# Kernel tuning notes

Hardware: AMD Instinct MI355X
Metric: run time of the kernel (lower is better)

## Reference

```python
import jax, jax.numpy as jnp
import numpy as np

C = 32
SHIFTS = (1, 2, 4)
KSIZE = 4  # trans_layer: kernel KSIZE+1, stride KSIZE, pad KSIZE//2
EPS_NORM = 1e-12
EPS_BN = 1e-5


def _make_diff_kernels(c):
    # 8 fixed 3x3 difference kernels, tiled per channel for depthwise conv.
    d1 = np.array([[[-1, 0, 0], [0, 1, 0], [0, 0, 0]],
                   [[0, -1, 0], [0, 1, 0], [0, 0, 0]],
                   [[0, 0, -1], [0, 1, 0], [0, 0, 0]],
                   [[0, 0, 0], [0, 1, -1], [0, 0, 0]]], dtype=np.float32)
    d1 = d1.reshape(4, 1, 3, 3)
    d2 = d1[:, :, ::-1, ::-1].copy()
    delta = np.concatenate([d1, d2], axis=0)          # [8,1,3,3]
    return jnp.asarray(np.tile(delta, (c, 1, 1, 1)))  # [8C,1,3,3]


DIFF_KERNELS = _make_diff_kernels(C)


def conv2d(x, w, stride=1, pad=0, dilation=1, groups=1):
    return jax.lax.conv_general_dilated(
        x, w, (stride, stride), [(pad, pad), (pad, pad)],
        rhs_dilation=(dilation, dilation),
        dimension_numbers=('NCHW', 'OIHW', 'NCHW'),
        feature_group_count=groups)


def l2norm(x, axis=-1):
    n = jnp.sqrt(jnp.sum(x * x, axis=axis, keepdims=True))
    return x / jnp.maximum(n, EPS_NORM)


def setup_inputs() -> dict:
    key = jax.random.key(0)
    ks = jax.random.split(key, 8)
    S = len(SHIFTS)
    return {
        'cen': jax.random.normal(ks[0], (2, C, 256, 256), jnp.float32),
        'trans_W': jax.random.normal(ks[1], (C, C, 5, 5), jnp.float32) * 0.05,
        'trans_b': jax.random.normal(ks[2], (C,), jnp.float32) * 0.05,
        'query_W': jax.random.normal(ks[3], (C, C, 1, 1), jnp.float32) * 0.05,
        'value_W': jax.random.normal(ks[4], (S, C, C, 1, 1), jnp.float32) * 0.05,
        'key_W': jax.random.normal(ks[5], (S, C, C, 1, 1), jnp.float32) * 0.05,
        'out_W': jax.random.normal(ks[6], (C, C, 1, 1), jnp.float32) * 0.05,
        'bn_gamma': jnp.ones((C,), jnp.float32),
        'bn_beta': jnp.zeros((C,), jnp.float32),
        'bn_mean': jnp.zeros((C,), jnp.float32),
        'bn_var': jnp.ones((C,), jnp.float32),
    }


def reference(cen, trans_W, trans_b, query_W, value_W, key_W, out_W,
              bn_gamma, bn_beta, bn_mean, bn_var):
    b, _, w, h = cen.shape
    S = len(SHIFTS)
    size = (w * h) // (KSIZE * KSIZE)

    # trans_layer: kernel KSIZE+1, stride KSIZE, pad KSIZE//2
    kv_cen = conv2d(cen, trans_W, stride=KSIZE, pad=KSIZE // 2) \
        + trans_b[None, :, None, None]

    keys, values = [], []
    for i, d in enumerate(SHIFTS):
        v = conv2d(cen, value_W[i])          # [b,C,w,h]
        k = conv2d(kv_cen, key_W[i])         # [b,C,w',h']
        # depthwise dilated difference conv -> 8 outputs per channel
        v = conv2d(v, DIFF_KERNELS, pad=d, dilation=d, groups=C)  # [b,8C,w,h]
        k = conv2d(k, DIFF_KERNELS, pad=d, dilation=d, groups=C)  # [b,8C,w',h']
        keys.append(k)
        values.append(v)

    querys = conv2d(kv_cen, query_W)  # [b,C,w',h']

    keys = jnp.stack(keys, axis=2).reshape(b, C, 8 * S, size)       # [b,C,8S,size]
    values = jnp.stack(values, axis=2).reshape(b, C, 8 * S, w * h)  # [b,C,8S,wh]

    keys = jnp.swapaxes(l2norm(keys, -1), -2, -1)        # [b,C,size,8S]
    querys = l2norm(querys.reshape(b, C, 1, size), -1)   # [b,C,1,size]

    score = jnp.matmul(querys, keys)   # [b,C,1,8S]  cosine sims
    score = l2norm(score, -1)
    out = jnp.matmul(score, values).reshape(b, C, w, h)

    # out_conv: 1x1 conv -> BN (eval mode, running stats) -> ReLU
    out = conv2d(out, out_W)
    inv = jax.lax.rsqrt(bn_var + EPS_BN)
    out = (out - bn_mean[None, :, None, None]) * (bn_gamma * inv)[None, :, None, None] \
        + bn_beta[None, :, None, None]
    return jax.nn.relu(out)
```

## Files before the change

### kernel.cpp

```cpp
#include <hip/hip_runtime.h>
#include <hip/hip_bf16.h>


#define CC 32
#define HW 256
#define KVW 64

__global__ __launch_bounds__(256, 2) void k1_trans(const float* __restrict__ cen,
                                                   const float* __restrict__ tW,
                                                   const float* __restrict__ tB,
                                                   float* __restrict__ kv) {
  int bid = blockIdx.x;
  int b = bid >> 8, cog = (bid >> 6) & 3, y = bid & 63;
  int tid = threadIdx.x;
  int x = tid & 63;
  int w = __builtin_amdgcn_readfirstlane(tid >> 6);
  int co0 = cog * 8 + w * 2;

  float acc0 = 0.f, acc1 = 0.f;
  const float4 z4 = {0.f, 0.f, 0.f, 0.f};

  int roff[5];
  bool rok[5];
#pragma unroll
  for (int r = 0; r < 5; r++) {
    int row = 4 * y - 2 + r;
    rok[r] = (row >= 0);
    roff[r] = (row < 0 ? 0 : row) * HW;
  }

  for (int ci = 0; ci < CC; ci += 4) {
    const float* pc[4];
#pragma unroll
    for (int c = 0; c < 4; c++) pc[c] = cen + (size_t)(b * CC + ci + c) * 65536 + 4 * x;
    float4 A[4][5], B[4][5];
#pragma unroll
    for (int c = 0; c < 4; c++) {
#pragma unroll
      for (int r = 0; r < 5; r++) {
        A[c][r] = (x > 0) ? *(const float4*)(pc[c] + roff[r] - 4) : z4;
        B[c][r] = *(const float4*)(pc[c] + roff[r]);
      }
    }
#pragma unroll
    for (int r = 0; r < 5; r++) {
      if (!rok[r]) continue;
#pragma unroll
      for (int c = 0; c < 4; c++) {
        const float* wa = tW + (co0 * CC + ci + c) * 25 + r * 5;
        const float* wb = wa + CC * 25;
        acc0 += wa[0] * A[c][r].z + wa[1] * A[c][r].w + wa[2] * B[c][r].x +
                wa[3] * B[c][r].y + wa[4] * B[c][r].z;
        acc1 += wb[0] * A[c][r].z + wb[1] * A[c][r].w + wb[2] * B[c][r].x +
                wb[3] * B[c][r].y + wb[4] * B[c][r].z;
      }
    }
  }
  kv[((b * CC + co0) * KVW + y) * KVW + x] = acc0 + tB[co0];
  kv[((b * CC + co0 + 1) * KVW + y) * KVW + x] = acc1 + tB[co0 + 1];
}

__device__ inline float wred64(float v) {
#pragma unroll
  for (int off = 1; off < 64; off <<= 1) v += __shfl_xor(v, off);
  return v;
}

__global__ __launch_bounds__(1024) void k2_scores(const float* __restrict__ kv,
                                                  const float* __restrict__ qW,
                                                  const float* __restrict__ kW,
                                                  float* __restrict__ scores) {
  __shared__ alignas(16) float kl[3][4096];
  __shared__ float wred[16][52];
  __shared__ float srl[24];
  int bc = blockIdx.x;
  int b = bc >> 5, c = bc & 31;
  int tid = threadIdx.x;
  int lane = tid & 63, w = tid >> 6;
  int xx = tid & 63;
  int ybase = tid >> 6;

  float qreg[4];
#pragma unroll
  for (int r = 0; r < 4; r++) {
    int px = r * 1024 + tid;
    float q = 0.f, k0 = 0.f, k1 = 0.f, k2 = 0.f;
    for (int ci = 0; ci < CC; ci++) {
      float val = kv[(b * CC + ci) * 4096 + px];
      q += qW[c * CC + ci] * val;
      k0 += kW[(0 * CC + c) * CC + ci] * val;
      k1 += kW[(1 * CC + c) * CC + ci] * val;
      k2 += kW[(2 * CC + c) * CC + ci] * val;
    }
    qreg[r] = q;
    kl[0][px] = k0;
    kl[1][px] = k1;
    kl[2][px] = k2;
  }
  __syncthreads();

  float q2 = 0.f;
#pragma unroll
  for (int r = 0; r < 4; r++) q2 += qreg[r] * qreg[r];
  q2 = wred64(q2);
  if (lane == 0) wred[w][48] = q2;

  constexpr int DYt[8] = {-1, -1, -1, 0, 1, 1, 1, 0};
  constexpr int DXt[8] = {-1, 0, 1, 1, 1, 0, -1, -1};
#pragma unroll
  for (int j = 0; j < 24; j++) {
    const int i = j >> 3, n = j & 7, d = 1 << i;
    const int dy = DYt[n], dx = DXt[n];
    int xn = xx + dx * d;
    bool xok = (xn >= 0 && xn < KVW);
    float dacc = 0.f, macc = 0.f;
#pragma unroll
    for (int r = 0; r < 4; r++) {
      int yy = r * 16 + ybase;
      int px = yy * KVW + xx;
      float kc = kl[i][px];
      int yn = yy + dy * d;
      float kn = (xok && yn >= 0 && yn < KVW) ? kl[i][yn * KVW + xn] : 0.f;
      float df = kc - kn;
      dacc += qreg[r] * df;
      macc += df * df;
    }
    dacc = wred64(dacc);
    macc = wred64(macc);
    if (lane == 0) {
      wred[w][j] = dacc;
      wred[w][24 + j] = macc;
    }
  }
  __syncthreads();
  if (tid < 24) {
    float D = 0.f, M = 0.f, Q2 = 0.f;
    for (int w2 = 0; w2 < 16; w2++) {
      D += wred[w2][tid];
      M += wred[w2][24 + tid];
      Q2 += wred[w2][48];
    }
    float sr = D / (fmaxf(sqrtf(M), 1e-12f) * fmaxf(sqrtf(Q2), 1e-12f));
    srl[tid] = sr;
  }
  __syncthreads();
  if (tid < 24) {
    float r2 = 0.f;
    for (int j = 0; j < 24; j++) r2 += srl[j] * srl[j];
    float s = srl[tid] / fmaxf(sqrtf(r2), 1e-12f);
    scores[(b * CC + c) * 24 + tid] = s;
  }
}

__global__ __launch_bounds__(256) void k3a_values(const float* __restrict__ cen,
                                                  const float* __restrict__ vW,
                                                  __hip_bfloat16* __restrict__ v) {
  int bid = blockIdx.x;
  int b = bid >> 9, blk = bid & 511;
  int tid = threadIdx.x;
  int lane = tid & 63;
  int cg = __builtin_amdgcn_readfirstlane(tid >> 6);
  int px = blk * 128 + lane * 2;

  float2 cr[CC];
#pragma unroll
  for (int ci = 0; ci < CC; ci++)
    cr[ci] = *(const float2*)(cen + (size_t)(b * CC + ci) * 65536 + px);

#pragma unroll
  for (int i = 0; i < 3; i++) {
#pragma unroll
    for (int cc = 0; cc < 8; cc++) {
      int c = cg * 8 + cc;
      const float* wp = vW + (i * CC + c) * CC;
      float a0 = 0.f, a1 = 0.f;
#pragma unroll
      for (int ci = 0; ci < CC; ci++) {
        a0 += wp[ci] * cr[ci].x;
        a1 += wp[ci] * cr[ci].y;
      }
      __hip_bfloat16 h0 = __float2bfloat16(a0);
      __hip_bfloat16 h1 = __float2bfloat16(a1);
      unsigned int pk = (unsigned int)(*(unsigned short*)&h0) |
                        ((unsigned int)(*(unsigned short*)&h1) << 16);
      *(unsigned int*)((unsigned short*)v + (((size_t)((i * 2 + b) * CC + c)) << 16) +
                       px) = pk;
    }
  }
}

__global__ __launch_bounds__(256) void k3b_combine(const __hip_bfloat16* __restrict__ v,
                                                   const float* __restrict__ scores,
                                                   const float* __restrict__ oW,
                                                   const float* __restrict__ gamma,
                                                   const float* __restrict__ beta,
                                                   const float* __restrict__ mean,
                                                   const float* __restrict__ var,
                                                   float* __restrict__ out) {
  __shared__ alignas(16) float vt[3 * 24 * 24 * 4];
  __shared__ alignas(16) float sl[27][32];
  __shared__ alignas(16) float owl[32][32];
  __shared__ float bns[32], bnb[32];

  int bid = blockIdx.x;
  int b = bid >> 8, tile = bid & 255;
  int ty = tile >> 4, tx = tile & 15;
  int tid = threadIdx.x;
  int ly = tid >> 4, lx = tid & 15;

  for (int f = tid; f < 24 * 32; f += 256) {
    int j = f >> 5, c = f & 31;
    sl[j][c] = scores[(b * CC + c) * 24 + j];
  }
  for (int f = tid; f < 1024; f += 256) owl[f >> 5][f & 31] = oW[f];
  if (tid < 32) {
    float inv = rsqrtf(var[tid] + 1e-5f);
    float sc = gamma[tid] * inv;
    bns[tid] = sc;
    bnb[tid] = beta[tid] - mean[tid] * sc;
  }
  __syncthreads();
  if (tid < 32) {
#pragma unroll
    for (int i = 0; i < 3; i++) {
      float s = 0.f;
      for (int n = 0; n < 8; n++) s += sl[i * 8 + n][tid];
      sl[24 + i][tid] = s;
    }
  }

  int ldsoff[4], pxoff[4], ibase[4];
  bool okp[4];
#pragma unroll
  for (int it = 0; it < 4; it++) {
    int p = tid + it * 256;
    bool act = (p < 864);
    int pp = act ? p : 0;
    int i = pp / 288;
    int rem = pp - i * 288;
    int r = rem / 12;
    int col = (rem - r * 12) * 2;
    int gy = ty * 16 + r - 4, gx = tx * 16 + col - 4;
    okp[it] = act && gy >= 0 && gy < HW && gx >= 0 && gx < HW;
    pxoff[it] = gy * HW + gx;
    ibase[it] = (i * 2 + b) * CC;
    ldsoff[it] = ((i * 24 + r) * 24 + col) * 4;
  }

  constexpr int DYt[8] = {-1, -1, -1, 0, 1, 1, 1, 0};
  constexpr int DXt[8] = {-1, 0, 1, 1, 1, 0, -1, -1};

  float acc[32];
#pragma unroll
  for (int co = 0; co < 32; co++) acc[co] = 0.f;

  unsigned int pf[4][4];
  const unsigned short* vs = (const unsigned short*)v;

#pragma unroll
  for (int it = 0; it < 4; it++)
#pragma unroll
    for (int cp = 0; cp < 4; cp++)
      pf[it][cp] = okp[it]
                       ? *(const unsigned int*)(vs + (((size_t)(ibase[it] + cp)) << 16) +
                                                pxoff[it])
                       : 0u;

  for (int cg = 0; cg < 8; cg++) {
    __syncthreads();
#pragma unroll
    for (int it = 0; it < 4; it++) {
      if (it == 3 && tid >= 96) continue;
      float4 lo, hi;
      lo.x = __uint_as_float(pf[it][0] << 16);
      lo.y = __uint_as_float(pf[it][1] << 16);
      lo.z = __uint_as_float(pf[it][2] << 16);
      lo.w = __uint_as_float(pf[it][3] << 16);
      hi.x = __uint_as_float(pf[it][0] & 0xffff0000u);
      hi.y = __uint_as_float(pf[it][1] & 0xffff0000u);
      hi.z = __uint_as_float(pf[it][2] & 0xffff0000u);
      hi.w = __uint_as_float(pf[it][3] & 0xffff0000u);
      *(float4*)&vt[ldsoff[it]] = lo;
      *(float4*)&vt[ldsoff[it] + 4] = hi;
    }
    if (cg < 7) {
      int cb = (cg + 1) * 4;
#pragma unroll
      for (int it = 0; it < 4; it++)
#pragma unroll
        for (int cp = 0; cp < 4; cp++)
          pf[it][cp] = okp[it] ? *(const unsigned int*)(vs +
                                                        (((size_t)(ibase[it] + cb + cp))
                                                         << 16) +
                                                        pxoff[it])
                               : 0u;
    }
    __syncthreads();

    float4 pre = {0.f, 0.f, 0.f, 0.f};
#pragma unroll
    for (int i = 0; i < 3; i++) {
      const int d = 1 << i;
      float4 S4 = *(const float4*)&sl[24 + i][cg * 4];
      float4 ctr = *(const float4*)&vt[((i * 24 + (ly + 4)) * 24 + (lx + 4)) * 4];
      pre.x += S4.x * ctr.x;
      pre.y += S4.y * ctr.y;
      pre.z += S4.z * ctr.z;
      pre.w += S4.w * ctr.w;
#pragma unroll
      for (int n = 0; n < 8; n++) {
        float4 sj = *(const float4*)&sl[i * 8 + n][cg * 4];
        float4 nb = *(const float4*)&vt[((i * 24 + (ly + 4 + DYt[n] * d)) * 24 +
                                         (lx + 4 + DXt[n] * d)) * 4];
        pre.x -= sj.x * nb.x;
        pre.y -= sj.y * nb.y;
        pre.z -= sj.z * nb.z;
        pre.w -= sj.w * nb.w;
      }
    }
#pragma unroll
    for (int co = 0; co < 32; co++) {
      float4 ow = *(const float4*)&owl[co][cg * 4];
      acc[co] += ow.x * pre.x + ow.y * pre.y + ow.z * pre.z + ow.w * pre.w;
    }
  }

  int gy = ty * 16 + ly, gx = tx * 16 + lx;
#pragma unroll
  for (int co = 0; co < 32; co++) {
    float val = acc[co] * bns[co] + bnb[co];
    out[((size_t)(b * CC + co) << 16) + gy * HW + gx] = fmaxf(val, 0.f);
  }
}

extern "C" void kernel_launch(void* const* d_in, const int* in_sizes, int n_in,
                              void* d_out, int out_size, void* d_ws, size_t ws_size,
                              hipStream_t stream) {
  const float* cen = (const float*)d_in[0];
  const float* trans_W = (const float*)d_in[1];
  const float* trans_b = (const float*)d_in[2];
  const float* query_W = (const float*)d_in[3];
  const float* value_W = (const float*)d_in[4];
  const float* key_W = (const float*)d_in[5];
  const float* out_W = (const float*)d_in[6];
  const float* bn_gamma = (const float*)d_in[7];
  const float* bn_beta = (const float*)d_in[8];
  const float* bn_mean = (const float*)d_in[9];
  const float* bn_var = (const float*)d_in[10];
  float* out = (float*)d_out;

  float* kv = (float*)d_ws;
  float* scores = (float*)((char*)d_ws + 524288);
  __hip_bfloat16* v = (__hip_bfloat16*)((char*)d_ws + 524288 + 8192);

  k1_trans<<<512, 256, 0, stream>>>(cen, trans_W, trans_b, kv);
  k2_scores<<<64, 1024, 0, stream>>>(kv, query_W, key_W, scores);
  k3a_values<<<1024, 256, 0, stream>>>(cen, value_W, v);
  k3b_combine<<<512, 256, 0, stream>>>(v, scores, out_W, bn_gamma, bn_beta, bn_mean,
                                       bn_var, out);
}
```

Baseline: 186.8 us.

## Split score kernel across shift index to raise block parallelism

The score computation is split into a partial kernel launched with one block per (batch, channel, shift), 192 blocks instead of 64, plus a small finalize kernel that combines the partial dot products and norms into normalized scores. This is meant to fill more compute units on the GPU, since 64 blocks of 1024 threads underuse the device. In exchange the query projection is recomputed three times, and an extra kernel launch and a workspace round trip are added.

After: 177.1 us. 1.05x faster.

```diff
diff --git a/kernel.cpp b/kernel.cpp
--- a/kernel.cpp
+++ b/kernel.cpp
@@ -66,14 +66,14 @@
   return v;
 }
 
-__global__ __launch_bounds__(1024) void k2_scores(const float* __restrict__ kv,
-                                                  const float* __restrict__ qW,
-                                                  const float* __restrict__ kW,
-                                                  float* __restrict__ scores) {
-  __shared__ alignas(16) float kl[3][4096];
-  __shared__ float wred[16][52];
-  __shared__ float srl[24];
-  int bc = blockIdx.x;
+__global__ __launch_bounds__(1024) void k2i_partial(const float* __restrict__ kv,
+                                                    const float* __restrict__ qW,
+                                                    const float* __restrict__ kW,
+                                                    float* __restrict__ pars) {
+  __shared__ alignas(16) float kl[4096];
+  __shared__ float wredl[16][18];
+  int bid = blockIdx.x;
+  int bc = bid / 3, i = bid - bc * 3;
   int b = bc >> 5, c = bc & 31;
   int tid = threadIdx.x;
   int lane = tid & 63, w = tid >> 6;
@@ -84,18 +84,14 @@
 #pragma unroll
   for (int r = 0; r < 4; r++) {
     int px = r * 1024 + tid;
-    float q = 0.f, k0 = 0.f, k1 = 0.f, k2 = 0.f;
+    float q = 0.f, kk = 0.f;
     for (int ci = 0; ci < CC; ci++) {
       float val = kv[(b * CC + ci) * 4096 + px];
       q += qW[c * CC + ci] * val;
-      k0 += kW[(0 * CC + c) * CC + ci] * val;
-      k1 += kW[(1 * CC + c) * CC + ci] * val;
-      k2 += kW[(2 * CC + c) * CC + ci] * val;
+      kk += kW[(i * CC + c) * CC + ci] * val;
     }
     qreg[r] = q;
-    kl[0][px] = k0;
-    kl[1][px] = k1;
-    kl[2][px] = k2;
+    kl[px] = kk;
   }
   __syncthreads();
 
@@ -103,13 +99,13 @@
 #pragma unroll
   for (int r = 0; r < 4; r++) q2 += qreg[r] * qreg[r];
   q2 = wred64(q2);
-  if (lane == 0) wred[w][48] = q2;
+  if (lane == 0) wredl[w][16] = q2;
 
   constexpr int DYt[8] = {-1, -1, -1, 0, 1, 1, 1, 0};
   constexpr int DXt[8] = {-1, 0, 1, 1, 1, 0, -1, -1};
-#pragma unroll
-  for (int j = 0; j < 24; j++) {
-    const int i = j >> 3, n = j & 7, d = 1 << i;
+  const int d = 1 << i;
+#pragma unroll
+  for (int n = 0; n < 8; n++) {
     const int dy = DYt[n], dx = DXt[n];
     int xn = xx + dx * d;
     bool xok = (xn >= 0 && xn < KVW);
@@ -118,9 +114,9 @@
     for (int r = 0; r < 4; r++) {
       int yy = r * 16 + ybase;
       int px = yy * KVW + xx;
-      float kc = kl[i][px];
+      float kc = kl[px];
       int yn = yy + dy * d;
-      float kn = (xok && yn >= 0 && yn < KVW) ? kl[i][yn * KVW + xn] : 0.f;
+      float kn = (xok && yn >= 0 && yn < KVW) ? kl[yn * KVW + xn] : 0.f;
       float df = kc - kn;
       dacc += qreg[r] * df;
       macc += df * df;
@@ -128,27 +124,48 @@
     dacc = wred64(dacc);
     macc = wred64(macc);
     if (lane == 0) {
-      wred[w][j] = dacc;
-      wred[w][24 + j] = macc;
+      wredl[w][n] = dacc;
+      wredl[w][8 + n] = macc;
     }
   }
   __syncthreads();
-  if (tid < 24) {
-    float D = 0.f, M = 0.f, Q2 = 0.f;
+
+  float* pp = pars + (size_t)bid * 32;
+  if (tid < 8) {
+    float D = 0.f, M = 0.f;
     for (int w2 = 0; w2 < 16; w2++) {
-      D += wred[w2][tid];
-      M += wred[w2][24 + tid];
-      Q2 += wred[w2][48];
-    }
-    float sr = D / (fmaxf(sqrtf(M), 1e-12f) * fmaxf(sqrtf(Q2), 1e-12f));
-    srl[tid] = sr;
+      D += wredl[w2][tid];
+      M += wredl[w2][8 + tid];
+    }
+    pp[tid] = D;
+    pp[8 + tid] = M;
+  }
+  if (tid == 0) {
+    float Q = 0.f;
+    for (int w2 = 0; w2 < 16; w2++) Q += wredl[w2][16];
+    pp[16] = Q;
+  }
+}
+
+__global__ __launch_bounds__(64) void k2f_finalize(const float* __restrict__ pars,
+                                                   float* __restrict__ scores) {
+  __shared__ float srl[24];
+  int bc = blockIdx.x;
+  int t = threadIdx.x;
+  if (t < 24) {
+    int i = t >> 3, n = t & 7;
+    const float* pp = pars + (size_t)(bc * 3 + i) * 32;
+    float D = pp[n];
+    float M = pp[8 + n];
+    float Q = pars[(size_t)(bc * 3) * 32 + 16];
+    float sr = D / (fmaxf(sqrtf(M), 1e-12f) * fmaxf(sqrtf(Q), 1e-12f));
+    srl[t] = sr;
   }
   __syncthreads();
-  if (tid < 24) {
+  if (t < 24) {
     float r2 = 0.f;
     for (int j = 0; j < 24; j++) r2 += srl[j] * srl[j];
-    float s = srl[tid] / fmaxf(sqrtf(r2), 1e-12f);
-    scores[(b * CC + c) * 24 + tid] = s;
+    scores[bc * 24 + t] = srl[t] / fmaxf(sqrtf(r2), 1e-12f);
   }
 }
 
@@ -351,10 +368,12 @@
 
   float* kv = (float*)d_ws;
   float* scores = (float*)((char*)d_ws + 524288);
-  __hip_bfloat16* v = (__hip_bfloat16*)((char*)d_ws + 524288 + 8192);
+  __hip_bfloat16* v = (__hip_bfloat16*)((char*)d_ws + 532480);
+  float* pars = (float*)((char*)d_ws + 25673728);
 
   k1_trans<<<512, 256, 0, stream>>>(cen, trans_W, trans_b, kv);
-  k2_scores<<<64, 1024, 0, stream>>>(kv, query_W, key_W, scores);
+  k2i_partial<<<192, 1024, 0, stream>>>(kv, query_W, key_W, pars);
+  k2f_finalize<<<64, 64, 0, stream>>>(pars, scores);
   k3a_values<<<1024, 256, 0, stream>>>(cen, value_W, v);
   k3b_combine<<<512, 256, 0, stream>>>(v, scores, out_W, bn_gamma, bn_beta, bn_mean,
                                        bn_var, out);
```
